# Performance work log

Measured on AMD Instinct MI355X. Metric: run time of the kernel, lower is better.

Reference implementation:

```python
import jax, jax.numpy as jnp
import numpy as np

N_NODES = 100000


def gcn_conv(x, row, col, norm, W, b):
    # PyG GCNConv: linear transform first, then normalized aggregation.
    h = x @ W                                   # [N, D_out]
    msg = h[col] * norm[:, None]                # gather sources, scale  [E', D_out]
    out = jax.ops.segment_sum(msg, row, num_segments=N_NODES)
    return out + b


def _build_norm(edge_index, n):
    # add self-loops
    loops = jnp.arange(n, dtype=edge_index.dtype)
    row = jnp.concatenate([edge_index[0], loops])  # targets
    col = jnp.concatenate([edge_index[1], loops])  # sources
    deg = jax.ops.segment_sum(jnp.ones(row.shape[0], jnp.float32), row, num_segments=n)
    dinv = jnp.where(deg > 0, jax.lax.rsqrt(deg), 0.0)
    norm = dinv[row] * dinv[col]
    return row, col, norm


def setup_inputs() -> dict:
    key = jax.random.key(0)
    k = jax.random.split(key, 5)
    N, E, IN, H, OUT = N_NODES, 1_600_000, 128, 64, 64
    x = jax.random.normal(k[0], (N, IN), jnp.float32)
    edge_index = jax.random.randint(k[1], (2, E), 0, N, dtype=jnp.int32)
    W1 = jax.random.normal(k[2], (IN, H), jnp.float32) / np.sqrt(IN)
    b1 = jnp.zeros((H,), jnp.float32)
    W2 = jax.random.normal(k[3], (H, OUT), jnp.float32) / np.sqrt(H)
    b2 = jnp.zeros((OUT,), jnp.float32)
    return {"x": x, "edge_index": edge_index, "W1": W1, "b1": b1, "W2": W2, "b2": b2}


def reference(x, edge_index, W1, b1, W2, b2):
    row, col, norm = _build_norm(edge_index, N_NODES)
    h = jax.nn.relu(gcn_conv(x, row, col, norm, W1, b1))
    # dropout is identity in eval mode
    out = gcn_conv(h, row, col, norm, W2, b2)
    return out
```

## Files before the change

kernel.cpp:

```cpp
#include <hip/hip_runtime.h>
#include <hip/hip_bf16.h>
#include <stdint.h>


#define BUCKET_CAP 64
#define NB_SHIFT 8
#define BIN_W (1 << NB_SHIFT)
#define EPB 8192

typedef __bf16 bf16x8 __attribute__((ext_vector_type(8)));
typedef float  f32x4  __attribute__((ext_vector_type(4)));

__device__ __forceinline__ void prep_w_one(const float* __restrict__ W,
                                           __bf16* __restrict__ Wsw, int t) {
    int lane = t & 63;
    int f = t >> 6;
    int kt = f >> 2, nt = f & 3;
    int k0 = kt * 32 + ((lane >> 4) * 8);
    int n  = nt * 16 + (lane & 15);
    __bf16* dst = Wsw + (size_t)t * 8;
#pragma unroll
    for (int j = 0; j < 8; ++j)
        dst[j] = (__bf16)W[(size_t)(k0 + j) * 64 + n];
}

__global__ void k_prep(const float* __restrict__ W1, const float* __restrict__ W2,
                       __bf16* __restrict__ W1sw, __bf16* __restrict__ W2sw,
                       int* __restrict__ bincnt, int NB) {
    int b = blockIdx.x;
    int tid = threadIdx.x;
    if (b < 4) {
        prep_w_one(W1, W1sw, b * 256 + tid);
    } else if (b < 6) {
        prep_w_one(W2, W2sw, (b - 4) * 256 + tid);
    } else {
        int i = (b - 6) * 256 + tid;
        if (i < NB) bincnt[i] = 0;
    }
}

__global__ void k_binA(const int* __restrict__ row, const int* __restrict__ col,
                       int E, int NB, int CAP,
                       int* __restrict__ bincnt, int* __restrict__ binbuf) {
    __shared__ int hist[512];
    __shared__ int base[512];
    int tid = threadIdx.x;
    int e0 = blockIdx.x * EPB;
    int eend = e0 + EPB; if (eend > E) eend = E;

    for (int i = tid; i < NB; i += 256) hist[i] = 0;
    __syncthreads();
    for (int e = e0 + tid; e < eend; e += 256)
        atomicAdd(&hist[((unsigned)row[e]) >> NB_SHIFT], 1);
    __syncthreads();
    for (int i = tid; i < NB; i += 256) {
        int h = hist[i];
        base[i] = h ? atomicAdd(&bincnt[i], h) : 0;
    }
    __syncthreads();
    for (int i = tid; i < NB; i += 256) hist[i] = 0;
    __syncthreads();
    for (int e = e0 + tid; e < eend; e += 256) {
        int r = row[e], c = col[e];
        int b = ((unsigned)r) >> NB_SHIFT;
        int p = atomicAdd(&hist[b], 1) + base[b];
        if (p < CAP)
            binbuf[(size_t)b * CAP + p] = (c << NB_SHIFT) | (r & (BIN_W - 1));
    }
}

__global__ void k_binB(const int* __restrict__ bincnt, const int* __restrict__ binbuf,
                       int CAP, int* __restrict__ cnt, float* __restrict__ dinv,
                       int* __restrict__ bucket, int N) {
    __shared__ int loc[BIN_W];
    int tid = threadIdx.x;
    int k = blockIdx.x;
    for (int i = tid; i < BIN_W; i += 256) loc[i] = 0;
    __syncthreads();
    int n_k = bincnt[k]; if (n_k > CAP) n_k = CAP;
    const int* buf = binbuf + (size_t)k * CAP;
    int node0 = k << NB_SHIFT;
    for (int i = tid; i < n_k; i += 256) {
        int v = buf[i];
        int rl = v & (BIN_W - 1);
        int c  = (int)(((unsigned)v) >> NB_SHIFT);
        int p = atomicAdd(&loc[rl], 1);
        if (p < BUCKET_CAP)
            bucket[(size_t)(node0 + rl) * BUCKET_CAP + p] = c;
    }
    __syncthreads();
    int node = node0 + tid;
    if (tid < BIN_W && node < N) {
        int d = loc[tid];
        cnt[node] = d;
        dinv[node] = rsqrtf((float)(d + 1));
    }
}

__global__ void k_gemm1(const float* __restrict__ X, const __bf16* __restrict__ W1sw,
                        __bf16* __restrict__ H1, int n_mtiles) {
    constexpr int KT = 4;
    constexpr int M_ITERS = 2;
    constexpr int KDIM = KT * 32;
    int lane = threadIdx.x & 63;
    int wave = threadIdx.x >> 6;
    int task = blockIdx.x * 4 + wave;
    int mt0 = task * M_ITERS;

    bf16x8 Bf[KT * 4];
    const bf16x8* Wv = (const bf16x8*)W1sw;
#pragma unroll
    for (int f = 0; f < KT * 4; ++f)
        Bf[f] = Wv[(size_t)f * 64 + lane];

    int m_in_tile = lane & 15;
    int k0 = (lane >> 4) * 8;

    for (int it = 0; it < M_ITERS; ++it) {
        int mt = mt0 + it;
        if (mt >= n_mtiles) return;
        int node = mt * 16 + m_in_tile;

        bf16x8 Af[KT];
#pragma unroll
        for (int kt = 0; kt < KT; ++kt) {
            const f32x4* p = (const f32x4*)(X + (size_t)node * KDIM + kt * 32 + k0);
            f32x4 lo = p[0], hi = p[1];
            bf16x8 a;
#pragma unroll
            for (int j = 0; j < 4; ++j) {
                a[j]     = (__bf16)lo[j];
                a[j + 4] = (__bf16)hi[j];
            }
            Af[kt] = a;
        }

#pragma unroll
        for (int nt = 0; nt < 4; ++nt) {
            f32x4 c = {0.f, 0.f, 0.f, 0.f};
#pragma unroll
            for (int kt = 0; kt < KT; ++kt)
                c = __builtin_amdgcn_mfma_f32_16x16x32_bf16(Af[kt], Bf[kt * 4 + nt], c, 0, 0, 0);
            int nd = mt * 16 + (lane >> 4) * 4;
            int ft = nt * 16 + (lane & 15);
#pragma unroll
            for (int r = 0; r < 4; ++r)
                H1[(size_t)(nd + r) * 64 + ft] = (__bf16)c[r];
        }
    }
}

__device__ __forceinline__ float gather_node_wide(const __bf16* __restrict__ H,
                                                  const int* __restrict__ cnt,
                                                  const float* __restrict__ dinv,
                                                  const int* __restrict__ bucket,
                                                  int node, int lane, float& di) {
    int deg = cnt[node];
    int m = deg > 63 ? 63 : deg;
    int   cj = (lane < m) ? bucket[(size_t)node * BUCKET_CAP + lane] : node;
    float dl = dinv[cj];
    float dj = (lane <= m) ? dl : 0.f;
    di = dinv[node];

    int r = lane >> 3, g = lane & 7;
    float acc8[8] = {0.f, 0.f, 0.f, 0.f, 0.f, 0.f, 0.f, 0.f};

#pragma unroll
    for (int j = 0; j < 32; j += 8) {
        int   c = __shfl(cj, j + r);
        float d = __shfl(dj, j + r);
        bf16x8 h = *(const bf16x8*)(H + (size_t)c * 64 + g * 8);
#pragma unroll
        for (int i = 0; i < 8; ++i)
            acc8[i] = fmaf(d, (float)h[i], acc8[i]);
    }
    int mp = m + 1;
    if (mp > 32) {
        for (int j = 32; j < mp; j += 8) {
            int   c = __shfl(cj, j + r);
            float d = __shfl(dj, j + r);
            bf16x8 h = *(const bf16x8*)(H + (size_t)c * 64 + g * 8);
#pragma unroll
            for (int i = 0; i < 8; ++i)
                acc8[i] = fmaf(d, (float)h[i], acc8[i]);
        }
    }

    bool b2 = (lane & 32) != 0;
    float a4[4];
#pragma unroll
    for (int i = 0; i < 4; ++i) {
        float send = b2 ? acc8[i] : acc8[i + 4];
        float keep = b2 ? acc8[i + 4] : acc8[i];
        a4[i] = keep + __shfl_xor(send, 32);
    }
    bool b1 = (lane & 16) != 0;
    float a2[2];
#pragma unroll
    for (int i = 0; i < 2; ++i) {
        float send = b1 ? a4[i] : a4[i + 2];
        float keep = b1 ? a4[i + 2] : a4[i];
        a2[i] = keep + __shfl_xor(send, 16);
    }
    bool b0 = (lane & 8) != 0;
    {
        float send = b0 ? a2[0] : a2[1];
        float keep = b0 ? a2[1] : a2[0];
        return keep + __shfl_xor(send, 8);
    }
}

__global__ void k_agg1_gemm2(const __bf16* __restrict__ H1, const int* __restrict__ cnt,
                             const float* __restrict__ dinv,
                             const int* __restrict__ bucket, const float* __restrict__ b1,
                             const __bf16* __restrict__ W2sw,
                             __bf16* __restrict__ H2, int N) {
    __shared__ __bf16 G1s[16][72];
    int lane = threadIdx.x & 63;
    int wave = threadIdx.x >> 6;
    int node0 = blockIdx.x * 16;
    int f = (lane & 7) * 8 + (lane >> 3);
    float bias = b1[f];

#pragma unroll
    for (int i = 0; i < 4; ++i) {
        int nrow = wave * 4 + i;
        int node = node0 + nrow;
        float v = 0.f;
        if (node < N) {
            float di;
            float s = gather_node_wide(H1, cnt, dinv, bucket, node, lane, di);
            v = fmaxf(fmaf(di, s, bias), 0.f);
        }
        G1s[nrow][f] = (__bf16)v;
    }
    __syncthreads();

    int m = lane & 15;
    int k0 = (lane >> 4) * 8;
    const bf16x8* Wv = (const bf16x8*)W2sw;
    bf16x8 Bf0 = Wv[(size_t)(0 * 4 + wave) * 64 + lane];
    bf16x8 Bf1 = Wv[(size_t)(1 * 4 + wave) * 64 + lane];
    bf16x8 Af0 = *(const bf16x8*)&G1s[m][k0];
    bf16x8 Af1 = *(const bf16x8*)&G1s[m][32 + k0];

    f32x4 c = {0.f, 0.f, 0.f, 0.f};
    c = __builtin_amdgcn_mfma_f32_16x16x32_bf16(Af0, Bf0, c, 0, 0, 0);
    c = __builtin_amdgcn_mfma_f32_16x16x32_bf16(Af1, Bf1, c, 0, 0, 0);

    int nd = node0 + (lane >> 4) * 4;
    int ft = wave * 16 + (lane & 15);
#pragma unroll
    for (int r = 0; r < 4; ++r)
        if (nd + r < N)
            H2[(size_t)(nd + r) * 64 + ft] = (__bf16)c[r];
}

__global__ void k_agg2(const __bf16* __restrict__ H2, const int* __restrict__ cnt,
                       const float* __restrict__ dinv,
                       const int* __restrict__ bucket, const float* __restrict__ b2,
                       float* __restrict__ out, int N) {
    int wave = threadIdx.x >> 6;
    int lane = threadIdx.x & 63;
    int node = blockIdx.x * 4 + wave;
    if (node >= N) return;
    int f = (lane & 7) * 8 + (lane >> 3);
    float di;
    float s = gather_node_wide(H2, cnt, dinv, bucket, node, lane, di);
    out[(size_t)node * 64 + f] = fmaf(di, s, b2[f]);
}

extern "C" void kernel_launch(void* const* d_in, const int* in_sizes, int n_in,
                              void* d_out, int out_size, void* d_ws, size_t ws_size,
                              hipStream_t stream) {
    (void)n_in; (void)out_size; (void)ws_size;
    const float* x  = (const float*)d_in[0];
    const int*   ei = (const int*)d_in[1];
    const float* W1 = (const float*)d_in[2];
    const float* b1 = (const float*)d_in[3];
    const float* W2 = (const float*)d_in[4];
    const float* b2 = (const float*)d_in[5];

    const int N = in_sizes[0] / 128;
    const int E = in_sizes[1] / 2;
    const int* row = ei;
    const int* col = ei + E;

    const int NB  = (N + BIN_W - 1) >> NB_SHIFT;
    const int CAP = 2 * ((E + NB - 1) / NB);

    char* ws = (char*)d_ws;
    size_t off = 0;
    auto take = [&](size_t bytes) -> char* {
        char* p = ws + off;
        off += (bytes + 255) & ~(size_t)255;
        return p;
    };
    int*    cnt    = (int*)   take((size_t)N * 4);
    float*  dinv   = (float*) take((size_t)N * 4);
    int*    bincnt = (int*)   take((size_t)NB * 4);
    int*    bucket = (int*)   take((size_t)N * BUCKET_CAP * 4);
    __bf16* W1sw   = (__bf16*)take((size_t)16 * 64 * 8 * 2);
    __bf16* W2sw   = (__bf16*)take((size_t)8  * 64 * 8 * 2);
    __bf16* H1     = (__bf16*)take((size_t)N * 64 * 2);
    size_t h2_bytes  = (size_t)N * 64 * 2;
    size_t bin_bytes = (size_t)NB * CAP * 4;
    char*   unionbuf = take(h2_bytes > bin_bytes ? h2_bytes : bin_bytes);
    int*    binbuf = (int*)unionbuf;
    __bf16* H2     = (__bf16*)unionbuf;

    const int n_mtiles = (N + 15) / 16;
    const int GB1 = (n_mtiles / 2 + 1 + 3) / 4;

    k_prep<<<6 + (NB + 255) / 256, 256, 0, stream>>>(W1, W2, W1sw, W2sw, bincnt, NB);
    k_binA<<<(E + EPB - 1) / EPB, 256, 0, stream>>>(row, col, E, NB, CAP, bincnt, binbuf);
    k_binB<<<NB, 256, 0, stream>>>(bincnt, binbuf, CAP, cnt, dinv, bucket, N);
    k_gemm1<<<GB1, 256, 0, stream>>>(x, W1sw, H1, n_mtiles);
    k_agg1_gemm2<<<(N + 15) / 16, 256, 0, stream>>>(H1, cnt, dinv, bucket, b1, W2sw, H2, N);
    k_agg2<<<(N + 3) / 4, 256, 0, stream>>>(H2, cnt, dinv, bucket, b2, (float*)d_out, N);
}
```

Measured before the change: 229.6 us.

## Merge binB with gemm1 launch, halve EPB, add low-degree gather fast path

```diff
diff --git a/kernel.cpp b/kernel.cpp
--- a/kernel.cpp
+++ b/kernel.cpp
@@ -6,7 +6,7 @@
 #define BUCKET_CAP 64
 #define NB_SHIFT 8
 #define BIN_W (1 << NB_SHIFT)
-#define EPB 8192
+#define EPB 4096
 
 typedef __bf16 bf16x8 __attribute__((ext_vector_type(8)));
 typedef float  f32x4  __attribute__((ext_vector_type(4)));
@@ -69,42 +69,43 @@
     }
 }
 
-__global__ void k_binB(const int* __restrict__ bincnt, const int* __restrict__ binbuf,
-                       int CAP, int* __restrict__ cnt, float* __restrict__ dinv,
-                       int* __restrict__ bucket, int N) {
+__global__ void k_binB_gemm1(const int* __restrict__ bincnt, const int* __restrict__ binbuf,
+                             int CAP, int* __restrict__ cnt, float* __restrict__ dinv,
+                             int* __restrict__ bucket, int N, int NB,
+                             const float* __restrict__ X, const __bf16* __restrict__ W1sw,
+                             __bf16* __restrict__ H1, int n_mtiles) {
     __shared__ int loc[BIN_W];
-    int tid = threadIdx.x;
-    int k = blockIdx.x;
-    for (int i = tid; i < BIN_W; i += 256) loc[i] = 0;
-    __syncthreads();
-    int n_k = bincnt[k]; if (n_k > CAP) n_k = CAP;
-    const int* buf = binbuf + (size_t)k * CAP;
-    int node0 = k << NB_SHIFT;
-    for (int i = tid; i < n_k; i += 256) {
-        int v = buf[i];
-        int rl = v & (BIN_W - 1);
-        int c  = (int)(((unsigned)v) >> NB_SHIFT);
-        int p = atomicAdd(&loc[rl], 1);
-        if (p < BUCKET_CAP)
-            bucket[(size_t)(node0 + rl) * BUCKET_CAP + p] = c;
-    }
-    __syncthreads();
-    int node = node0 + tid;
-    if (tid < BIN_W && node < N) {
-        int d = loc[tid];
-        cnt[node] = d;
-        dinv[node] = rsqrtf((float)(d + 1));
-    }
-}
-
-__global__ void k_gemm1(const float* __restrict__ X, const __bf16* __restrict__ W1sw,
-                        __bf16* __restrict__ H1, int n_mtiles) {
+    if (blockIdx.x < (unsigned)NB) {
+        int tid = threadIdx.x;
+        int k = blockIdx.x;
+        for (int i = tid; i < BIN_W; i += 256) loc[i] = 0;
+        __syncthreads();
+        int n_k = bincnt[k]; if (n_k > CAP) n_k = CAP;
+        const int* buf = binbuf + (size_t)k * CAP;
+        int node0 = k << NB_SHIFT;
+        for (int i = tid; i < n_k; i += 256) {
+            int v = buf[i];
+            int rl = v & (BIN_W - 1);
+            int c  = (int)(((unsigned)v) >> NB_SHIFT);
+            int p = atomicAdd(&loc[rl], 1);
+            if (p < BUCKET_CAP)
+                bucket[(size_t)(node0 + rl) * BUCKET_CAP + p] = c;
+        }
+        __syncthreads();
+        int node = node0 + tid;
+        if (tid < BIN_W && node < N) {
+            int d = loc[tid];
+            cnt[node] = d;
+            dinv[node] = rsqrtf((float)(d + 1));
+        }
+        return;
+    }
     constexpr int KT = 4;
     constexpr int M_ITERS = 2;
     constexpr int KDIM = KT * 32;
     int lane = threadIdx.x & 63;
     int wave = threadIdx.x >> 6;
-    int task = blockIdx.x * 4 + wave;
+    int task = (blockIdx.x - NB) * 4 + wave;
     int mt0 = task * M_ITERS;
 
     bf16x8 Bf[KT * 4];
@@ -164,25 +165,44 @@
 
     int r = lane >> 3, g = lane & 7;
     float acc8[8] = {0.f, 0.f, 0.f, 0.f, 0.f, 0.f, 0.f, 0.f};
-
-#pragma unroll
-    for (int j = 0; j < 32; j += 8) {
-        int   c = __shfl(cj, j + r);
-        float d = __shfl(dj, j + r);
-        bf16x8 h = *(const bf16x8*)(H + (size_t)c * 64 + g * 8);
-#pragma unroll
-        for (int i = 0; i < 8; ++i)
-            acc8[i] = fmaf(d, (float)h[i], acc8[i]);
-    }
     int mp = m + 1;
-    if (mp > 32) {
-        for (int j = 32; j < mp; j += 8) {
+
+    if (mp <= 16) {
+#pragma unroll
+        for (int j = 0; j < 16; j += 8) {
             int   c = __shfl(cj, j + r);
             float d = __shfl(dj, j + r);
             bf16x8 h = *(const bf16x8*)(H + (size_t)c * 64 + g * 8);
 #pragma unroll
             for (int i = 0; i < 8; ++i)
                 acc8[i] = fmaf(d, (float)h[i], acc8[i]);
+        }
+    } else {
+#pragma unroll
+        for (int j = 0; j < 32; j += 8) {
+            int   c = __shfl(cj, j + r);
+            float d = __shfl(dj, j + r);
+            bf16x8 h = *(const bf16x8*)(H + (size_t)c * 64 + g * 8);
+#pragma unroll
+            for (int i = 0; i < 8; ++i)
+                acc8[i] = fmaf(d, (float)h[i], acc8[i]);
+        }
+        if (mp > 32) {
+#pragma unroll 1
+            for (int j = 32; j < mp; j += 16) {
+                int   c0 = __shfl(cj, j + r);
+                float d0 = __shfl(dj, j + r);
+                int   c1 = __shfl(cj, j + 8 + r);
+                float d1 = __shfl(dj, j + 8 + r);
+                bf16x8 h0 = *(const bf16x8*)(H + (size_t)c0 * 64 + g * 8);
+                bf16x8 h1 = *(const bf16x8*)(H + (size_t)c1 * 64 + g * 8);
+#pragma unroll
+                for (int i = 0; i < 8; ++i)
+                    acc8[i] = fmaf(d0, (float)h0[i], acc8[i]);
+#pragma unroll
+                for (int i = 0; i < 8; ++i)
+                    acc8[i] = fmaf(d1, (float)h1[i], acc8[i]);
+            }
         }
     }
 
@@ -314,8 +334,8 @@
 
     k_prep<<<6 + (NB + 255) / 256, 256, 0, stream>>>(W1, W2, W1sw, W2sw, bincnt, NB);
     k_binA<<<(E + EPB - 1) / EPB, 256, 0, stream>>>(row, col, E, NB, CAP, bincnt, binbuf);
-    k_binB<<<NB, 256, 0, stream>>>(bincnt, binbuf, CAP, cnt, dinv, bucket, N);
-    k_gemm1<<<GB1, 256, 0, stream>>>(x, W1sw, H1, n_mtiles);
+    k_binB_gemm1<<<NB + GB1, 256, 0, stream>>>(bincnt, binbuf, CAP, cnt, dinv, bucket,
+                                               N, NB, x, W1sw, H1, n_mtiles);
     k_agg1_gemm2<<<(N + 15) / 16, 256, 0, stream>>>(H1, cnt, dinv, bucket, b1, W2sw, H2, N);
     k_agg2<<<(N + 3) / 4, 256, 0, stream>>>(H2, cnt, dinv, bucket, b2, (float*)d_out, N);
 }
```

After: 236.8 us. 1.03x slower.
